# Performance work log

Hardware: AMD Instinct MI355X
Metric: run time of the kernel (lower is better)

Reference implementation:

```python
import jax, jax.numpy as jnp
import numpy as np

T = 35        # points per voxel
D, H, W = 10, 400, 352  # voxel grid (KITTI car setting)
EPS = 1e-5    # BatchNorm eps


def setup_inputs() -> dict:
    key = jax.random.key(0)
    ks = jax.random.split(key, 10)
    K = 15000  # non-empty voxels in the frame
    feature = jax.random.normal(ks[0], (K, T, 7), jnp.float32)
    # realistic padding: each voxel has 5..35 valid points, rest zero
    npts = jax.random.randint(ks[1], (K,), 5, T + 1)
    valid = jnp.arange(T)[None, :] < npts[:, None]
    feature = feature * valid[:, :, None].astype(jnp.float32)
    c_b = jnp.zeros((K, 1), jnp.int32)
    c_d = jax.random.randint(ks[2], (K, 1), 0, D).astype(jnp.int32)
    c_h = jax.random.randint(ks[3], (K, 1), 0, H).astype(jnp.int32)
    c_w = jax.random.randint(ks[4], (K, 1), 0, W).astype(jnp.int32)
    coordinate = jnp.concatenate([c_b, c_d, c_h, c_w], axis=1)
    W1 = jax.random.normal(ks[5], (7, 16), jnp.float32) * 0.1
    b1 = jnp.zeros((16,), jnp.float32)
    g1 = jnp.ones((16,), jnp.float32)
    be1 = jnp.zeros((16,), jnp.float32)
    W2 = jax.random.normal(ks[6], (32, 64), jnp.float32) * 0.1
    b2 = jnp.zeros((64,), jnp.float32)
    g2 = jnp.ones((64,), jnp.float32)
    be2 = jnp.zeros((64,), jnp.float32)
    return {"feature": feature, "coordinate": coordinate, "bs": 1,
            "W1": W1, "b1": b1, "g1": g1, "be1": be1,
            "W2": W2, "b2": b2, "g2": g2, "be2": be2}


def _vfe(x, mask, Wm, b, g, be):
    # Linear + ReLU per point: [K, T, cin] -> [K, T, cmid]
    pw = jax.nn.relu(jnp.einsum('ktc,cd->ktd', x, Wm) + b)
    # BatchNorm1d (training mode): per-channel stats over (K, T), biased var
    mu = pw.mean(axis=(0, 1))
    var = pw.var(axis=(0, 1))
    pw = (pw - mu) * jax.lax.rsqrt(var + EPS) * g + be
    # max over points, broadcast-concat (VoxelNet VFE)
    agg = pw.max(axis=1, keepdims=True)               # [K, 1, cmid]
    cat = jnp.concatenate([pw, jnp.broadcast_to(agg, pw.shape)], axis=-1)
    return cat * mask  # mask padded points


def reference(feature, coordinate, bs, W1, b1, g1, be1, W2, b2, g2, be2):
    # mask: point is valid if its channel-wise max != 0 (as in original)
    vmax = feature.max(axis=2, keepdims=True)          # [K, T, 1]
    mask = (vmax != 0).astype(feature.dtype)
    x = _vfe(feature, mask, W1, b1, g1, be1)           # [K, T, 32]
    x = _vfe(x, mask, W2, b2, g2, be2)                 # [K, T, 128]
    voxelwise = x.max(axis=1)                          # [K, 128]
    # scatter into dense grid (sparse COO -> to_dense sums duplicates)
    out = jnp.zeros((bs, D, H, W, 128), feature.dtype)
    out = out.at[coordinate[:, 0], coordinate[:, 1],
                 coordinate[:, 2], coordinate[:, 3]].add(voxelwise)
    return out
```

## Files before the change

### kernel.cpp

```cpp
#include <hip/hip_runtime.h>
#include <math.h>

#define KVOX 15000
#define TP 35
#define CIN 7
#define CM1 16
#define CM2 64
#define NPTS (KVOX * TP)
#define DD 10
#define HH 400
#define WWID 352
#define EPSBN 1e-5f
#define NB1 1024
#define NBV 3750

__global__ __launch_bounds__(256) void stats1_kernel(
    const float* __restrict__ feat, const float* __restrict__ W1,
    const float* __restrict__ b1, float* __restrict__ partial1)
{
    __shared__ float w1s[CIN * CM1];
    __shared__ float b1s[CM1];
    __shared__ float red[4][32];
    int tid = threadIdx.x;
    if (tid < CIN * CM1) w1s[tid] = W1[tid];
    if (tid < CM1) b1s[tid] = b1[tid];
    __syncthreads();

    float s[CM1], q[CM1];
#pragma unroll
    for (int c = 0; c < CM1; ++c) { s[c] = 0.f; q[c] = 0.f; }

    for (int i = blockIdx.x * 256 + tid; i < NPTS; i += NB1 * 256) {
        float f[CIN];
#pragma unroll
        for (int j = 0; j < CIN; ++j) f[j] = feat[(size_t)i * CIN + j];
#pragma unroll
        for (int c = 0; c < CM1; ++c) {
            float acc = b1s[c];
#pragma unroll
            for (int j = 0; j < CIN; ++j) acc = fmaf(f[j], w1s[j * CM1 + c], acc);
            float pw = fmaxf(acc, 0.f);
            s[c] += pw; q[c] += pw * pw;
        }
    }
#pragma unroll
    for (int c = 0; c < CM1; ++c) {
#pragma unroll
        for (int off = 32; off > 0; off >>= 1) {
            s[c] += __shfl_xor(s[c], off);
            q[c] += __shfl_xor(q[c], off);
        }
    }
    int wid = tid >> 6, lane = tid & 63;
    if (lane == 0) {
#pragma unroll
        for (int c = 0; c < CM1; ++c) { red[wid][c] = s[c]; red[wid][CM1 + c] = q[c]; }
    }
    __syncthreads();
    if (tid < 32)
        partial1[blockIdx.x * 32 + tid] =
            red[0][tid] + red[1][tid] + red[2][tid] + red[3][tid];
}

__global__ __launch_bounds__(256) void reduce1_kernel(
    const float* __restrict__ partial1, const float* __restrict__ g1,
    const float* __restrict__ be1, float* __restrict__ coef1)
{
    __shared__ float acc[8][32];
    __shared__ float tot[32];
    int tid = threadIdx.x;
    int c = tid & 31, part = tid >> 5;
    float v = 0.f;
    for (int b = part; b < NB1; b += 8) v += partial1[b * 32 + c];
    acc[part][c] = v;
    __syncthreads();
    if (tid < 32) {
        float t = 0.f;
#pragma unroll
        for (int p = 0; p < 8; ++p) t += acc[p][tid];
        tot[tid] = t;
    }
    __syncthreads();
    if (tid < CM1) {
        float inv = 1.f / (float)NPTS;
        float mu = tot[tid] * inv;
        float var = tot[CM1 + tid] * inv - mu * mu;
        float a = g1[tid] * rsqrtf(var + EPSBN);
        coef1[tid] = a;
        coef1[CM1 + tid] = be1[tid] - mu * a;
    }
}

template <bool FINAL>
__global__ __launch_bounds__(256) void vfe_kernel(
    const float* __restrict__ feat,
    const float* __restrict__ W1g, const float* __restrict__ b1g,
    const float* __restrict__ coef1,
    const float* __restrict__ W2g, const float* __restrict__ b2g,
    const float* __restrict__ coef2,
    const int*  __restrict__ coord,
    float* __restrict__ partial2,
    float* __restrict__ out)
{
    __shared__ float sfeat[4][TP * CIN + 11];
    alignas(16) __shared__ float scat[4][TP * 32];
    __shared__ float smask[4][TP + 5];
    __shared__ float red2[4][2 * CM2];

    int tid = threadIdx.x, wid = tid >> 6, lane = tid & 63;
    int k = blockIdx.x * 4 + wid;
    int tg = lane >> 4, c1 = lane & 15;

    float w1r[CIN];
#pragma unroll
    for (int j = 0; j < CIN; ++j) w1r[j] = W1g[j * CM1 + c1];
    float b1r = b1g[c1];
    float a1r = coef1[c1], d1r = coef1[CM1 + c1];
    float w2r[32];
#pragma unroll
    for (int j = 0; j < 32; ++j) w2r[j] = W2g[j * CM2 + lane];
    float b2r = b2g[lane];
    float a2r = 0.f, d2r = 0.f;
    if constexpr (FINAL) { a2r = coef2[lane]; d2r = coef2[CM2 + lane]; }

    float* F = sfeat[wid];
    float* CT = scat[wid];
    float* M = smask[wid];

    for (int i = lane; i < TP * CIN; i += 64)
        F[i] = feat[(size_t)k * (TP * CIN) + i];
    __syncthreads();

    float maxv = -INFINITY;
#pragma unroll
    for (int it = 0; it < 9; ++it) {
        int t = tg + 4 * it;
        if (t < TP) {
            float fv0 = F[t * CIN];
            float m7 = fv0;
            float acc = fmaf(fv0, w1r[0], b1r);
#pragma unroll
            for (int j = 1; j < CIN; ++j) {
                float fv = F[t * CIN + j];
                m7 = fmaxf(m7, fv);
                acc = fmaf(fv, w1r[j], acc);
            }
            float maskv = (m7 != 0.f) ? 1.f : 0.f;
            float pw = fmaxf(acc, 0.f);
            float bn = fmaf(pw, a1r, d1r);
            maxv = fmaxf(maxv, bn);
            CT[t * 32 + c1] = bn * maskv;
            if (c1 == 0) M[t] = maskv;
        }
    }
    maxv = fmaxf(maxv, __shfl_xor(maxv, 16));
    maxv = fmaxf(maxv, __shfl_xor(maxv, 32));
#pragma unroll
    for (int it = 0; it < 9; ++it) {
        int t = tg + 4 * it;
        if (t < TP) CT[t * 32 + 16 + c1] = maxv * M[t];
    }

    float s_acc = 0.f, q_acc = 0.f;
    float agg2 = -INFINITY, v1 = -INFINITY, mmin = 1.f;
    for (int t = 0; t < TP; ++t) {
        const float4* r4 = reinterpret_cast<const float4*>(&CT[t * 32]);
        float acc0 = b2r, acc1 = 0.f;
#pragma unroll
        for (int i = 0; i < 8; i += 2) {
            float4 va = r4[i], vb = r4[i + 1];
            acc0 = fmaf(va.x, w2r[4 * i + 0], acc0);
            acc0 = fmaf(va.y, w2r[4 * i + 1], acc0);
            acc0 = fmaf(va.z, w2r[4 * i + 2], acc0);
            acc0 = fmaf(va.w, w2r[4 * i + 3], acc0);
            acc1 = fmaf(vb.x, w2r[4 * i + 4], acc1);
            acc1 = fmaf(vb.y, w2r[4 * i + 5], acc1);
            acc1 = fmaf(vb.z, w2r[4 * i + 6], acc1);
            acc1 = fmaf(vb.w, w2r[4 * i + 7], acc1);
        }
        float pw = fmaxf(acc0 + acc1, 0.f);
        if constexpr (!FINAL) {
            s_acc += pw; q_acc += pw * pw;
        } else {
            float bn = fmaf(pw, a2r, d2r);
            agg2 = fmaxf(agg2, bn);
            float mk = M[t];
            v1 = fmaxf(v1, bn * mk);
            mmin = fminf(mmin, mk);
        }
    }

    if constexpr (!FINAL) {
        red2[wid][lane] = s_acc;
        red2[wid][CM2 + lane] = q_acc;
        __syncthreads();
        if (tid < 2 * CM2)
            partial2[(size_t)blockIdx.x * (2 * CM2) + tid] =
                red2[0][tid] + red2[1][tid] + red2[2][tid] + red2[3][tid];
    } else {
        float v2 = (mmin == 0.f) ? fmaxf(agg2, 0.f) : agg2;
        int cd = coord[k * 4 + 1], ch = coord[k * 4 + 2], cw = coord[k * 4 + 3];
        size_t base = ((((size_t)cd * HH) + ch) * WWID + cw) * 128;
        atomicAdd(&out[base + lane], v1);
        atomicAdd(&out[base + 64 + lane], v2);
    }
}

__global__ __launch_bounds__(1024) void reduce2_kernel(
    const float* __restrict__ partial2, const float* __restrict__ g2,
    const float* __restrict__ be2, float* __restrict__ coef2)
{
    __shared__ float acc[8][128];
    __shared__ float tot[128];
    int tid = threadIdx.x;
    int c = tid & 127, part = tid >> 7;
    float v = 0.f;
    for (int b = part; b < NBV; b += 8) v += partial2[(size_t)b * 128 + c];
    acc[part][c] = v;
    __syncthreads();
    if (tid < 128) {
        float t = 0.f;
#pragma unroll
        for (int p = 0; p < 8; ++p) t += acc[p][tid];
        tot[tid] = t;
    }
    __syncthreads();
    if (tid < CM2) {
        float inv = 1.f / (float)NPTS;
        float mu = tot[tid] * inv;
        float var = tot[CM2 + tid] * inv - mu * mu;
        float a = g2[tid] * rsqrtf(var + EPSBN);
        coef2[tid] = a;
        coef2[CM2 + tid] = be2[tid] - mu * a;
    }
}

extern "C" void kernel_launch(void* const* d_in, const int* in_sizes, int n_in,
                              void* d_out, int out_size, void* d_ws, size_t ws_size,
                              hipStream_t stream)
{
    const float* feat = (const float*)d_in[0];
    const int*   coord = (const int*)d_in[1];
    const float* W1  = (const float*)d_in[3];
    const float* b1  = (const float*)d_in[4];
    const float* g1  = (const float*)d_in[5];
    const float* be1 = (const float*)d_in[6];
    const float* W2  = (const float*)d_in[7];
    const float* b2  = (const float*)d_in[8];
    const float* g2  = (const float*)d_in[9];
    const float* be2 = (const float*)d_in[10];
    float* out = (float*)d_out;

    float* wsf = (float*)d_ws;
    float* partial1 = wsf;
    float* partial2 = wsf + 32768;
    float* coef1 = wsf + 32768 + 480000;
    float* coef2 = coef1 + 32;

    hipMemsetAsync(d_out, 0, (size_t)out_size * sizeof(float), stream);

    stats1_kernel<<<NB1, 256, 0, stream>>>(feat, W1, b1, partial1);
    reduce1_kernel<<<1, 256, 0, stream>>>(partial1, g1, be1, coef1);
    vfe_kernel<false><<<NBV, 256, 0, stream>>>(feat, W1, b1, coef1, W2, b2,
                                               nullptr, nullptr, partial2, nullptr);
    reduce2_kernel<<<1, 1024, 0, stream>>>(partial2, g2, be2, coef2);
    vfe_kernel<true><<<NBV, 256, 0, stream>>>(feat, W1, b1, coef1, W2, b2,
                                              coef2, coord, nullptr, out);
}
```

Measured before the change: 966.7 us.

## Replace dense memset plus scatter atomics with compact buffer and single gather-write pass

Builds a cell-to-voxel lookup table via atomicMin, accumulates voxel features into a compact buffer instead of the dense grid, then writes the whole dense output in one vectorized pass that fills zeros or copies voxel data. This removes the separate memset followed by scattered atomics into the large output. It also parallelizes the second BN statistics reduction across channels and shrinks the first stats grid. The cost is extra table initialization and reads over all grid cells.

Result: faster. 935.7 us (-3.2%).

```diff
diff --git a/kernel.cpp b/kernel.cpp
--- a/kernel.cpp
+++ b/kernel.cpp
@@ -10,13 +10,32 @@
 #define DD 10
 #define HH 400
 #define WWID 352
+#define NCELL (DD * HH * WWID)
 #define EPSBN 1e-5f
-#define NB1 1024
+#define NB1 256
 #define NBV 3750
 
+typedef float vfloat4 __attribute__((ext_vector_type(4)));
+typedef int   vint4   __attribute__((ext_vector_type(4)));
+
+#define NT4 (NCELL / 4)
+#define NC4 (KVOX * 128 / 4)
+#define NBI ((NT4 + NC4 + 255) / 256)
+__global__ __launch_bounds__(256) void init_kernel(vint4* __restrict__ table4,
+                                                   vfloat4* __restrict__ comp4)
+{
+    int i = blockIdx.x * 256 + threadIdx.x;
+    if (i < NT4) {
+        table4[i] = (vint4){0x7FFFFFFF, 0x7FFFFFFF, 0x7FFFFFFF, 0x7FFFFFFF};
+    } else if (i - NT4 < NC4) {
+        comp4[i - NT4] = (vfloat4){0.f, 0.f, 0.f, 0.f};
+    }
+}
+
 __global__ __launch_bounds__(256) void stats1_kernel(
-    const float* __restrict__ feat, const float* __restrict__ W1,
-    const float* __restrict__ b1, float* __restrict__ partial1)
+    const float* __restrict__ feat, const int* __restrict__ coord,
+    const float* __restrict__ W1, const float* __restrict__ b1,
+    float* __restrict__ partial1, int* __restrict__ table)
 {
     __shared__ float w1s[CIN * CM1];
     __shared__ float b1s[CM1];
@@ -24,6 +43,12 @@
     int tid = threadIdx.x;
     if (tid < CIN * CM1) w1s[tid] = W1[tid];
     if (tid < CM1) b1s[tid] = b1[tid];
+
+    int g = blockIdx.x * 256 + tid;
+    if (g < KVOX) {
+        int cell = (coord[g * 4 + 1] * HH + coord[g * 4 + 2]) * WWID + coord[g * 4 + 3];
+        atomicMin(&table[cell], g);
+    }
     __syncthreads();
 
     float s[CM1], q[CM1];
@@ -99,8 +124,9 @@
     const float* __restrict__ W2g, const float* __restrict__ b2g,
     const float* __restrict__ coef2,
     const int*  __restrict__ coord,
+    const int*  __restrict__ table,
     float* __restrict__ partial2,
-    float* __restrict__ out)
+    float* __restrict__ compact)
 {
     __shared__ float sfeat[4][TP * CIN + 11];
     alignas(16) __shared__ float scat[4][TP * 32];
@@ -199,39 +225,63 @@
                 red2[0][tid] + red2[1][tid] + red2[2][tid] + red2[3][tid];
     } else {
         float v2 = (mmin == 0.f) ? fmaxf(agg2, 0.f) : agg2;
-        int cd = coord[k * 4 + 1], ch = coord[k * 4 + 2], cw = coord[k * 4 + 3];
-        size_t base = ((((size_t)cd * HH) + ch) * WWID + cw) * 128;
-        atomicAdd(&out[base + lane], v1);
-        atomicAdd(&out[base + 64 + lane], v2);
-    }
-}
-
-__global__ __launch_bounds__(1024) void reduce2_kernel(
+        int cell = (coord[k * 4 + 1] * HH + coord[k * 4 + 2]) * WWID + coord[k * 4 + 3];
+        int w = table[cell];
+        atomicAdd(&compact[(size_t)w * 128 + lane], v1);
+        atomicAdd(&compact[(size_t)w * 128 + 64 + lane], v2);
+    }
+}
+
+__global__ __launch_bounds__(256) void reduce2_kernel(
     const float* __restrict__ partial2, const float* __restrict__ g2,
     const float* __restrict__ be2, float* __restrict__ coef2)
 {
-    __shared__ float acc[8][128];
-    __shared__ float tot[128];
+    __shared__ float sred[4][2];
+    int c = blockIdx.x;
     int tid = threadIdx.x;
-    int c = tid & 127, part = tid >> 7;
-    float v = 0.f;
-    for (int b = part; b < NBV; b += 8) v += partial2[(size_t)b * 128 + c];
-    acc[part][c] = v;
-    __syncthreads();
-    if (tid < 128) {
-        float t = 0.f;
-#pragma unroll
-        for (int p = 0; p < 8; ++p) t += acc[p][tid];
-        tot[tid] = t;
-    }
-    __syncthreads();
-    if (tid < CM2) {
+    float s = 0.f, q = 0.f;
+    for (int r = tid; r < NBV; r += 256) {
+        s += partial2[(size_t)r * 128 + c];
+        q += partial2[(size_t)r * 128 + CM2 + c];
+    }
+#pragma unroll
+    for (int off = 32; off > 0; off >>= 1) {
+        s += __shfl_xor(s, off);
+        q += __shfl_xor(q, off);
+    }
+    int wid = tid >> 6;
+    if ((tid & 63) == 0) { sred[wid][0] = s; sred[wid][1] = q; }
+    __syncthreads();
+    if (tid == 0) {
+        float S = sred[0][0] + sred[1][0] + sred[2][0] + sred[3][0];
+        float Q = sred[0][1] + sred[1][1] + sred[2][1] + sred[3][1];
         float inv = 1.f / (float)NPTS;
-        float mu = tot[tid] * inv;
-        float var = tot[CM2 + tid] * inv - mu * mu;
-        float a = g2[tid] * rsqrtf(var + EPSBN);
-        coef2[tid] = a;
-        coef2[CM2 + tid] = be2[tid] - mu * a;
+        float mu = S * inv;
+        float var = Q * inv - mu * mu;
+        float a = g2[c] * rsqrtf(var + EPSBN);
+        coef2[c] = a;
+        coef2[CM2 + c] = be2[c] - mu * a;
+    }
+}
+
+#define NWT (NCELL * 32 / 4)
+#define NBW (NWT / 256)
+__global__ __launch_bounds__(256) void write_kernel(
+    vfloat4* __restrict__ out, const int* __restrict__ table,
+    const float* __restrict__ compact)
+{
+    int t = blockIdx.x * 256 + threadIdx.x;
+    size_t f4 = (size_t)t * 4;
+    int cell = (int)(f4 >> 5);
+    int w = table[cell];
+    if (w < KVOX) {
+        const vfloat4* src =
+            reinterpret_cast<const vfloat4*>(&compact[(size_t)w * 128 + ((f4 & 31) << 2)]);
+        out[f4 + 0] = src[0]; out[f4 + 1] = src[1];
+        out[f4 + 2] = src[2]; out[f4 + 3] = src[3];
+    } else {
+        const vfloat4 z = {0.f, 0.f, 0.f, 0.f};
+        out[f4 + 0] = z; out[f4 + 1] = z; out[f4 + 2] = z; out[f4 + 3] = z;
     }
 }
 
@@ -251,19 +301,22 @@
     const float* be2 = (const float*)d_in[10];
     float* out = (float*)d_out;
 
-    float* wsf = (float*)d_ws;
-    float* partial1 = wsf;
-    float* partial2 = wsf + 32768;
-    float* coef1 = wsf + 32768 + 480000;
-    float* coef2 = coef1 + 32;
-
-    hipMemsetAsync(d_out, 0, (size_t)out_size * sizeof(float), stream);
-
-    stats1_kernel<<<NB1, 256, 0, stream>>>(feat, W1, b1, partial1);
+    int*   table    = (int*)d_ws;
+    float* compact  = (float*)d_ws + NCELL;
+    float* partial1 = compact + KVOX * 128;
+    float* partial2 = partial1 + NB1 * 32;
+    float* coef1    = partial2 + NBV * 128;
+    float* coef2    = coef1 + 32;
+
+    init_kernel<<<NBI, 256, 0, stream>>>((vint4*)table, (vfloat4*)compact);
+    stats1_kernel<<<NB1, 256, 0, stream>>>(feat, coord, W1, b1, partial1, table);
     reduce1_kernel<<<1, 256, 0, stream>>>(partial1, g1, be1, coef1);
     vfe_kernel<false><<<NBV, 256, 0, stream>>>(feat, W1, b1, coef1, W2, b2,
-                                               nullptr, nullptr, partial2, nullptr);
-    reduce2_kernel<<<1, 1024, 0, stream>>>(partial2, g2, be2, coef2);
+                                               nullptr, nullptr, nullptr,
+                                               partial2, nullptr);
+    reduce2_kernel<<<CM2, 256, 0, stream>>>(partial2, g2, be2, coef2);
     vfe_kernel<true><<<NBV, 256, 0, stream>>>(feat, W1, b1, coef1, W2, b2,
-                                              coef2, coord, nullptr, out);
-}
+                                              coef2, coord, table,
+                                              nullptr, compact);
+    write_kernel<<<NBW, 256, 0, stream>>>((vfloat4*)out, table, compact);
+}
```
